# Performance work log

Hardware: AMD Instinct MI355X
Metric: run time of the kernel (lower is better)

The kernel has to match this reference:

```python
import jax, jax.numpy as jnp
import numpy as np

N = 4000; T_GRU = 32; T_TREE = 16; F = 256; HS = 128; H = 3 * HS; CC = 512; E = 64000; D4 = 4 * HS


def _gru_last(x, wi, wh, bi, bh):
    # x: [N, T, F]; torch GRU gate order r, z, n. Returns last hidden [N, H].
    xp = jnp.einsum('ntf,gf->ntg', x, wi) + bi  # [N, T, 3H]
    h0 = jnp.zeros((x.shape[0], wh.shape[1]), x.dtype)
    def step(h, xt):
        gh = h @ wh.T + bh
        ir, iz, inn = jnp.split(xt, 3, axis=1)
        hr, hz, hn = jnp.split(gh, 3, axis=1)
        r = jax.nn.sigmoid(ir + hr)
        z = jax.nn.sigmoid(iz + hz)
        n = jnp.tanh(inn + r * hn)
        return (1.0 - z) * n + z * h, None
    hT, _ = jax.lax.scan(step, h0, jnp.swapaxes(xp, 0, 1))
    return hT


def _tree_root(x, ioux_w, ioux_b, iouh_w, iouh_b, fx_w, fx_b, fh_w, fh_b):
    # Chain-structured TreeLSTM (each node has one child); x: [N, T, F], leaf-to-root.
    xi = jnp.einsum('ntf,gf->ntg', x, ioux_w) + ioux_b  # [N, T, 3M]
    xf = jnp.einsum('ntf,mf->ntm', x, fx_w) + fx_b      # [N, T, M]
    M = fh_w.shape[0]
    z0 = jnp.zeros((x.shape[0], M), x.dtype)
    def step(carry, xs):
        c, h = carry
        xi_t, xf_t = xs
        iou = xi_t + h @ iouh_w.T + iouh_b
        i, o, u = jnp.split(iou, 3, axis=1)
        f = jax.nn.sigmoid(xf_t + h @ fh_w.T + fh_b)
        c = jax.nn.sigmoid(i) * jnp.tanh(u) + f * c
        h = jax.nn.sigmoid(o) * jnp.tanh(c)
        return (c, h), None
    (c, h), _ = jax.lax.scan(step, (z0, z0), (jnp.swapaxes(xi, 0, 1), jnp.swapaxes(xf, 0, 1)))
    return h


def _gcn(x, w, b, row, col):
    # PyG GCNConv: self-loops + symmetric normalization.
    n = x.shape[0]
    xw = x @ w.T
    loops = jnp.arange(n, dtype=row.dtype)
    r = jnp.concatenate([row, loops])
    c = jnp.concatenate([col, loops])
    deg = jax.ops.segment_sum(jnp.ones(r.shape, x.dtype), c, num_segments=n)
    dinv = jnp.where(deg > 0, jax.lax.rsqrt(jnp.maximum(deg, 1e-12)), 0.0)
    norm = (dinv[r] * dinv[c])[:, None]
    return jax.ops.segment_sum(xw[r] * norm, c, num_segments=n) + b


def setup_inputs() -> dict:
    key = jax.random.key(0)
    ks = jax.random.split(key, 48)
    s = 0.05
    p = lambda i, sh: jax.random.normal(ks[i], sh, jnp.float32) * s
    return {
        'feat1': p(0, (N, T_GRU, F)),
        'feat2': p(1, (N, T_TREE, F)),
        'feat3': p(2, (N, T_TREE, F)),
        'feat4': p(3, (N, CC)),
        'edge_index': jax.random.randint(ks[4], (2, E), 0, N),
        'gru_wi': p(5, (3 * H, F)), 'gru_wh': p(6, (3 * H, H)),
        'gru_bi': p(7, (3 * H,)), 'gru_bh': p(8, (3 * H,)),
        't1_ioux_w': p(9, (3 * H, F)), 't1_ioux_b': p(10, (3 * H,)),
        't1_iouh_w': p(11, (3 * H, H)), 't1_iouh_b': p(12, (3 * H,)),
        't1_fx_w': p(13, (H, F)), 't1_fx_b': p(14, (H,)),
        't1_fh_w': p(15, (H, H)), 't1_fh_b': p(16, (H,)),
        't2_ioux_w': p(17, (3 * H, F)), 't2_ioux_b': p(18, (3 * H,)),
        't2_iouh_w': p(19, (3 * H, H)), 't2_iouh_b': p(20, (3 * H,)),
        't2_fx_w': p(21, (H, F)), 't2_fx_b': p(22, (H,)),
        't2_fh_w': p(23, (H, H)), 't2_fh_b': p(24, (H,)),
        'r1_w': p(25, (HS, H)), 'r1_b': p(26, (HS,)),
        'r2_w': p(27, (HS, H)), 'r2_b': p(28, (HS,)),
        'r3_w': p(29, (HS, H)), 'r3_b': p(30, (HS,)),
        'r4_w': p(31, (HS, CC)), 'r4_b': p(32, (HS,)),
        'gcn0_w': p(33, (D4, D4)), 'gcn0_b': p(34, (D4,)),
        'gcn1_w': p(35, (D4, D4)), 'gcn1_b': p(36, (D4,)),
        'r7_w': p(37, (2, D4)), 'r7_b': p(38, (2,)),
    }


def reference(feat1, feat2, feat3, feat4, edge_index,
              gru_wi, gru_wh, gru_bi, gru_bh,
              t1_ioux_w, t1_ioux_b, t1_iouh_w, t1_iouh_b, t1_fx_w, t1_fx_b, t1_fh_w, t1_fh_b,
              t2_ioux_w, t2_ioux_b, t2_iouh_w, t2_iouh_b, t2_fx_w, t2_fx_b, t2_fh_w, t2_fh_b,
              r1_w, r1_b, r2_w, r2_b, r3_w, r3_b, r4_w, r4_b,
              gcn0_w, gcn0_b, gcn1_w, gcn1_b, r7_w, r7_b):
    v1 = _gru_last(feat1, gru_wi, gru_wh, gru_bi, gru_bh)            # [N, H]
    v2 = _tree_root(feat2, t1_ioux_w, t1_ioux_b, t1_iouh_w, t1_iouh_b, t1_fx_w, t1_fx_b, t1_fh_w, t1_fh_b)
    v3 = _tree_root(feat3, t2_ioux_w, t2_ioux_b, t2_iouh_w, t2_iouh_b, t2_fx_w, t2_fx_b, t2_fh_w, t2_fh_b)
    f1 = v1 @ r1_w.T + r1_b
    f2 = v2 @ r2_w.T + r2_b
    f3 = v3 @ r3_w.T + r3_b
    f4 = feat4 @ r4_w.T + r4_b
    m = jnp.concatenate([f1, f2, f3, f4], axis=1)                    # [N, 4*HS]
    row, col = edge_index[0], edge_index[1]
    m = jax.nn.relu(_gcn(m, gcn0_w, gcn0_b, row, col))
    m = _gcn(m, gcn1_w, gcn1_b, row, col)
    m = jax.nn.softmax(m @ r7_w.T + r7_b, axis=1)                    # [N, 2]
    return m.T                                                       # [2, N]
```

## Files before the change

kernel.cpp:

```cpp
#include <hip/hip_runtime.h>
#include <hip/hip_bf16.h>
#include <math.h>

#define NN 4000
#define TG 32
#define TT 16
#define FF 256
#define HH 384
#define GCOLS 1536
#define KCAT 640
#define EE 64000
#define D4 512

typedef __attribute__((ext_vector_type(8))) short short8;
typedef __attribute__((ext_vector_type(4))) float float4v;

static __device__ __forceinline__ float fsig(float x)  { return 1.0f / (1.0f + __expf(-x)); }
static __device__ __forceinline__ float ftanh(float x) { return 2.0f / (1.0f + __expf(-2.0f*x)) - 1.0f; }
static __device__ __forceinline__ unsigned short f2bf(float f) {
    __hip_bfloat16 h = __float2bfloat16(f); return *reinterpret_cast<unsigned short*>(&h);
}

static __device__ __forceinline__ void async_copy16(const void* g, void* l) {
    __builtin_amdgcn_global_load_lds(
        (const __attribute__((address_space(1))) unsigned int*)g,
        (__attribute__((address_space(3))) unsigned int*)l, 16, 0, 0);
}

static __device__ __forceinline__ void xcd_swz(int& bx, int& by, int& bz) {
    const int gx = gridDim.x, gy = gridDim.y;
    const int nwg = gx * gy * gridDim.z;
    const int w = (blockIdx.z * gy + blockIdx.y) * gx + blockIdx.x;
    const int q = nwg >> 3, r = nwg & 7;
    const int xcd = w & 7, i = w >> 3;
    const int L = (xcd < r ? xcd*(q+1) : r*(q+1) + (xcd - r)*q) + i;
    bx = L % gx; int rest = L / gx;
    by = rest % gy; bz = rest / gy;
}

__global__ __launch_bounds__(256) void prep_w_kernel(
    const float* __restrict__ gwi, const float* __restrict__ gwh,
    const float* __restrict__ gbi, const float* __restrict__ gbh,
    const float* __restrict__ x1w, const float* __restrict__ x1b,
    const float* __restrict__ h1w, const float* __restrict__ h1b,
    const float* __restrict__ fx1w, const float* __restrict__ fx1b,
    const float* __restrict__ fh1w, const float* __restrict__ fh1b,
    const float* __restrict__ x2w, const float* __restrict__ x2b,
    const float* __restrict__ h2w, const float* __restrict__ h2b,
    const float* __restrict__ fx2w, const float* __restrict__ fx2b,
    const float* __restrict__ fh2w, const float* __restrict__ fh2b,
    __hip_bfloat16* __restrict__ Wx, __hip_bfloat16* __restrict__ Wh,
    float* __restrict__ bp)
{
    int z = blockIdx.z;
    int idx = blockIdx.x * 256 + threadIdx.x;
    int c = idx / KCAT, k = idx - c * KCAT;
    int bx = c >> 7, wc = (c >> 6) & 1, g = (c >> 4) & 3, rl = c & 15;
    int j = bx*32 + wc*16 + rl;
    float v = 0.0f, bv = 0.0f;
    if (z == 0) {
        if (g <= 1) {
            int row = g*HH + j;
            v = (k < FF) ? gwi[row*FF + k] : gwh[row*HH + (k-FF)];
            bv = gbi[row] + gbh[row];
        } else if (g == 2) {
            int row = 2*HH + j;
            v = (k < FF) ? gwi[row*FF + k] : 0.0f;
            bv = gbi[row];
        } else {
            int row = 2*HH + j;
            v = (k < FF) ? 0.0f : gwh[row*HH + (k-FF)];
            bv = gbh[row];
        }
    } else {
        const float* xw  = (z==1)? x1w  : x2w;   const float* xb  = (z==1)? x1b  : x2b;
        const float* hw  = (z==1)? h1w  : h2w;   const float* hb_ = (z==1)? h1b  : h2b;
        const float* fxw = (z==1)? fx1w : fx2w;  const float* fxb = (z==1)? fx1b : fx2b;
        const float* fhw = (z==1)? fh1w : fh2w;  const float* fhb = (z==1)? fh1b : fh2b;
        if (g < 3) {
            int row = g*HH + j;
            v = (k < FF) ? xw[row*FF + k] : hw[row*HH + (k-FF)];
            bv = xb[row] + hb_[row];
        } else {
            v = (k < FF) ? fxw[j*FF + k] : fhw[j*HH + (k-FF)];
            bv = fxb[j] + fhb[j];
        }
    }
    if (k < FF) Wx[(size_t)z*GCOLS*FF + (size_t)c*FF + k] = __float2bfloat16(v);
    else        Wh[(size_t)z*GCOLS*HH + (size_t)c*HH + (k-FF)] = __float2bfloat16(v);
    if (k == 0) bp[z*GCOLS + c] = bv;
}

__global__ __launch_bounds__(256) void f2b4_kernel(const float* __restrict__ s,
                                                   __hip_bfloat16* __restrict__ d, int n4)
{
    int i = blockIdx.x*256 + threadIdx.x;
    if (i >= n4) return;
    float4 v = ((const float4*)s)[i];
    ushort4 u = { f2bf(v.x), f2bf(v.y), f2bf(v.z), f2bf(v.w) };
    ((ushort4*)d)[i] = u;
}

#define BM 128
#define BN 128
#define BKK 32

__global__ __launch_bounds__(256) void gemm0_k(
    const __hip_bfloat16* __restrict__ Ab, size_t zA, int lda,
    const __hip_bfloat16* __restrict__ Wb, size_t zW, int K,
    const float* __restrict__ bias, size_t zB,
    float* __restrict__ C, size_t zC,
    __hip_bfloat16* __restrict__ C16, size_t zC16,
    int ldC, int M)
{
    const int z = blockIdx.z;
    const __hip_bfloat16* A = Ab + zA*z;
    const __hip_bfloat16* W = Wb + zW*z;

    __shared__ __align__(16) __hip_bfloat16 As[BM][BKK];
    __shared__ __align__(16) __hip_bfloat16 Bs[BN][BKK];

    const int tid  = threadIdx.x;
    const int lane = tid & 63;
    const int w    = tid >> 6;
    const int wr = w >> 1, wc = w & 1;
    const int rowBase = blockIdx.y * BM;
    const int colBase = blockIdx.x * BN;
    const int sRow = tid >> 2;
    const int sK   = (tid & 3) * 8;

    float4v acc[4][4];
    #pragma unroll
    for (int i = 0; i < 4; ++i)
        #pragma unroll
        for (int j = 0; j < 4; ++j)
            acc[i][j] = (float4v){0.f, 0.f, 0.f, 0.f};

    const int rl = lane & 15;
    const int kl = (lane >> 4) * 8;

    for (int kt = 0; kt < K; kt += BKK) {
        const int kk = kt + sK;
        #pragma unroll
        for (int i = 0; i < 2; ++i) {
            int gr = rowBase + i*64 + sRow;
            if (gr > M-1) gr = M-1;
            async_copy16(A + (size_t)gr*lda + kk, &As[i*64 + sRow][sK]);
        }
        #pragma unroll
        for (int i = 0; i < 2; ++i) {
            int r = i*64 + sRow;
            async_copy16(W + (size_t)(colBase + r)*K + kk, &Bs[r][sK]);
        }
        __syncthreads();

        short8 af[4], bfr[4];
        #pragma unroll
        for (int mi = 0; mi < 4; ++mi)
            af[mi] = *(const short8*)&As[wr*64 + mi*16 + rl][kl];
        #pragma unroll
        for (int ni = 0; ni < 4; ++ni)
            bfr[ni] = *(const short8*)&Bs[wc*64 + ni*16 + rl][kl];
        #pragma unroll
        for (int mi = 0; mi < 4; ++mi)
            #pragma unroll
            for (int ni = 0; ni < 4; ++ni)
                acc[mi][ni] = __builtin_amdgcn_mfma_f32_16x16x32_bf16(af[mi], bfr[ni], acc[mi][ni], 0, 0, 0);
        __syncthreads();
    }

    const int rq = (lane >> 4) * 4;
    float* Cz = C + zC*z;
    __hip_bfloat16* C16z = C16 ? (C16 + zC16*z) : nullptr;
    #pragma unroll
    for (int mi = 0; mi < 4; ++mi) {
        #pragma unroll
        for (int q = 0; q < 4; ++q) {
            int row = rowBase + wr*64 + mi*16 + rq + q;
            if (row >= M) continue;
            #pragma unroll
            for (int ni = 0; ni < 4; ++ni) {
                int col = colBase + wc*64 + ni*16 + rl;
                float v = acc[mi][ni][q];
                if (bias) v += bias[zB*z + col];
                Cz[(size_t)row*ldC + col] = v;
                if (C16z) C16z[(size_t)row*ldC + col] = __float2bfloat16(v);
            }
        }
    }
}

struct StepSet {
    const __hip_bfloat16 *X, *Hin, *Wx, *Wh;
    const float *bp, *Sin;
    float *Sout;
    __hip_bfloat16 *Hout;
    int lda, xoff;
};

#define NT (KCAT/BKK)
#define SBM 64

template<int MODE>
__global__ __launch_bounds__(256) void step_k(StepSet S)
{
    int bxi, byi, bzi;
    xcd_swz(bxi, byi, bzi);

    const __hip_bfloat16* X  = S.X;
    const __hip_bfloat16* Hi = S.Hin;
    const __hip_bfloat16* Wx = S.Wx;
    const __hip_bfloat16* Wh = S.Wh;
    const float* bp = S.bp;
    const float* Si = S.Sin;
    float* So = S.Sout;
    __hip_bfloat16* Ho = S.Hout;
    const int lda = S.lda, xoff = S.xoff;

    __shared__ __align__(16) __hip_bfloat16 As[4][SBM][BKK];
    __shared__ __align__(16) __hip_bfloat16 Bs[4][BN][BKK];

    const int tid  = threadIdx.x;
    const int lane = tid & 63;
    const int w    = tid >> 6;
    const int wr = w >> 1, wc = w & 1;
    const int rowBase = byi * SBM;
    const int colBase = bxi * BN;

    const int sR  = tid >> 2;
    const int sC  = tid & 3;
    const int sSw = sC ^ ((sR >> 1) & 3);
    int gra = rowBase + sR; if (gra > NN-1) gra = NN-1;

    auto stage = [&](int buf, int kt) {
        if (kt < FF) {
            const int kk = kt + sSw*8;
            async_copy16(X  + (size_t)gra*lda + xoff + kk,          &As[buf][sR][sC*8]);
            async_copy16(Wx + (size_t)(colBase + sR)*FF + kk,       &Bs[buf][sR][sC*8]);
            async_copy16(Wx + (size_t)(colBase + 64 + sR)*FF + kk,  &Bs[buf][64 + sR][sC*8]);
        } else {
            const int kk = kt - FF + sSw*8;
            async_copy16(Hi + (size_t)gra*HH + kk,                  &As[buf][sR][sC*8]);
            async_copy16(Wh + (size_t)(colBase + sR)*HH + kk,       &Bs[buf][sR][sC*8]);
            async_copy16(Wh + (size_t)(colBase + 64 + sR)*HH + kk,  &Bs[buf][64 + sR][sC*8]);
        }
    };

    float4v acc[2][4];
    #pragma unroll
    for (int i = 0; i < 2; ++i)
        #pragma unroll
        for (int j = 0; j < 4; ++j)
            acc[i][j] = (float4v){0.f, 0.f, 0.f, 0.f};

    const int rl = lane & 15;
    const int dF = (lane >> 4) ^ ((rl >> 1) & 3);

    stage(0, 0);
    stage(1, BKK);

    for (int it = 0; it < NT; ++it) {
        if (it < NT-1) asm volatile("s_waitcnt vmcnt(3)" ::: "memory");
        else           asm volatile("s_waitcnt vmcnt(0)" ::: "memory");
        __builtin_amdgcn_sched_barrier(0);
        __builtin_amdgcn_s_barrier();
        __builtin_amdgcn_sched_barrier(0);
        if (it + 2 < NT) stage((it+2)&3, (it+2)*BKK);
        __builtin_amdgcn_sched_barrier(0);

        const int cur = it & 3;
        short8 af[2], bfr[4];
        #pragma unroll
        for (int mi = 0; mi < 2; ++mi)
            af[mi] = *(const short8*)&As[cur][wr*32 + mi*16 + rl][dF*8];

        const bool xph = (it*BKK) < FF;
        if (MODE == 2) {
            #pragma unroll
            for (int ni = 0; ni < 4; ++ni)
                bfr[ni] = *(const short8*)&Bs[cur][wc*64 + ni*16 + rl][dF*8];
            asm volatile("s_waitcnt lgkmcnt(0)" ::: "memory");
            __builtin_amdgcn_sched_barrier(0);
            #pragma unroll
            for (int mi = 0; mi < 2; ++mi)
                #pragma unroll
                for (int ni = 0; ni < 4; ++ni)
                    acc[mi][ni] = __builtin_amdgcn_mfma_f32_16x16x32_bf16(af[mi], bfr[ni], acc[mi][ni], 0, 0, 0);
        } else if (xph) {
            #pragma unroll
            for (int ni = 0; ni < 3; ++ni)
                bfr[ni] = *(const short8*)&Bs[cur][wc*64 + ni*16 + rl][dF*8];
            asm volatile("s_waitcnt lgkmcnt(0)" ::: "memory");
            __builtin_amdgcn_sched_barrier(0);
            #pragma unroll
            for (int mi = 0; mi < 2; ++mi)
                #pragma unroll
                for (int ni = 0; ni < 3; ++ni)
                    acc[mi][ni] = __builtin_amdgcn_mfma_f32_16x16x32_bf16(af[mi], bfr[ni], acc[mi][ni], 0, 0, 0);
        } else {
            bfr[0] = *(const short8*)&Bs[cur][wc*64 + 0*16 + rl][dF*8];
            bfr[1] = *(const short8*)&Bs[cur][wc*64 + 1*16 + rl][dF*8];
            bfr[3] = *(const short8*)&Bs[cur][wc*64 + 3*16 + rl][dF*8];
            asm volatile("s_waitcnt lgkmcnt(0)" ::: "memory");
            __builtin_amdgcn_sched_barrier(0);
            #pragma unroll
            for (int mi = 0; mi < 2; ++mi) {
                acc[mi][0] = __builtin_amdgcn_mfma_f32_16x16x32_bf16(af[mi], bfr[0], acc[mi][0], 0, 0, 0);
                acc[mi][1] = __builtin_amdgcn_mfma_f32_16x16x32_bf16(af[mi], bfr[1], acc[mi][1], 0, 0, 0);
                acc[mi][3] = __builtin_amdgcn_mfma_f32_16x16x32_bf16(af[mi], bfr[3], acc[mi][3], 0, 0, 0);
            }
        }
    }

    const int rq = (lane >> 4) * 4;
    const int j  = (colBase >> 2) + wc*16 + rl;
    const int cb = colBase + wc*64 + rl;
    float b0 = bp[cb + 0];
    float b1 = bp[cb + 16];
    float b2 = bp[cb + 32];
    float b3 = bp[cb + 48];

    #pragma unroll
    for (int mi = 0; mi < 2; ++mi) {
        #pragma unroll
        for (int q = 0; q < 4; ++q) {
            int row = rowBase + wr*32 + mi*16 + rq + q;
            if (row >= NN) continue;
            float g0 = acc[mi][0][q] + b0;
            float g1 = acc[mi][1][q] + b1;
            float g2 = acc[mi][2][q] + b2;
            float g3 = acc[mi][3][q] + b3;
            size_t off = (size_t)row*HH + j;
            if (MODE == 1) {
                float r  = fsig(g0), zz = fsig(g1);
                float n  = ftanh(g2 + r*g3);
                float hp = Si[off];
                float hn = (1.0f - zz)*n + zz*hp;
                So[off] = hn;
                Ho[off] = __float2bfloat16(hn);
            } else {
                float cp = Si[off];
                float cn = fsig(g0)*ftanh(g2) + fsig(g3)*cp;
                So[off] = cn;
                float hn = fsig(g1)*ftanh(cn);
                Ho[off] = __float2bfloat16(hn);
            }
        }
    }
}

__global__ __launch_bounds__(256) void count_kernel(const int* __restrict__ col, int* __restrict__ degi)
{
    int e = blockIdx.x*256 + threadIdx.x;
    if (e < EE) atomicAdd(&degi[col[e]], 1);
}

__global__ __launch_bounds__(1024) void scan_kernel(const int* __restrict__ degi,
    int* __restrict__ start, int* __restrict__ cursor, float* __restrict__ dinv)
{
    __shared__ int s[1024];
    int t = threadIdx.x;
    int v[4]; int sum = 0;
    #pragma unroll
    for (int i = 0; i < 4; ++i) {
        int idx = t*4 + i;
        v[i] = (idx < NN) ? degi[idx] : 0;
        sum += v[i];
    }
    s[t] = sum;
    __syncthreads();
    for (int d = 1; d < 1024; d <<= 1) {
        int x = (t >= d) ? s[t-d] : 0;
        __syncthreads();
        s[t] += x;
        __syncthreads();
    }
    int base = s[t] - sum;
    int run = 0;
    #pragma unroll
    for (int i = 0; i < 4; ++i) {
        int idx = t*4 + i;
        if (idx < NN) {
            int st = base + run;
            start[idx] = st;
            cursor[idx] = st;
            dinv[idx] = rsqrtf((float)v[i] + 1.0f);
        }
        run += v[i];
    }
    if (t == 1023) start[NN] = s[1023];
}

__global__ __launch_bounds__(256) void fill_kernel(const int* __restrict__ row,
    const int* __restrict__ col, int* __restrict__ cursor, int* __restrict__ esrc)
{
    int e = blockIdx.x*256 + threadIdx.x;
    if (e < EE) {
        int c = col[e];
        int pos = atomicAdd(&cursor[c], 1);
        esrc[pos] = row[e];
    }
}

__global__ __launch_bounds__(256) void gather_kernel(const float* __restrict__ xw,
    const int* __restrict__ esrc, const int* __restrict__ start,
    const float* __restrict__ dinv, const float* __restrict__ bias,
    float* __restrict__ mout, __hip_bfloat16* __restrict__ mout16, int relu)
{
    int wv = threadIdx.x >> 6, lane = threadIdx.x & 63;
    int n = blockIdx.x*4 + wv;
    if (n >= NN) return;
    float a[8] = {0.f,0.f,0.f,0.f,0.f,0.f,0.f,0.f};
    int s0 = start[n], s1 = start[n+1];
    float dn = dinv[n];
    for (int e = s0; e < s1; ++e) {
        int r = esrc[e];
        float nrm = dinv[r]*dn;
        const float4 v0 = *(const float4*)(xw + (size_t)r*D4 + lane*8);
        const float4 v1 = *(const float4*)(xw + (size_t)r*D4 + lane*8 + 4);
        a[0] += v0.x*nrm; a[1] += v0.y*nrm; a[2] += v0.z*nrm; a[3] += v0.w*nrm;
        a[4] += v1.x*nrm; a[5] += v1.y*nrm; a[6] += v1.z*nrm; a[7] += v1.w*nrm;
    }
    const float4 u0 = *(const float4*)(xw + (size_t)n*D4 + lane*8);
    const float4 u1 = *(const float4*)(xw + (size_t)n*D4 + lane*8 + 4);
    float dd = dn*dn;
    float su[8] = {u0.x,u0.y,u0.z,u0.w,u1.x,u1.y,u1.z,u1.w};
    #pragma unroll
    for (int i = 0; i < 8; ++i) {
        float vv = a[i] + su[i]*dd + bias[lane*8 + i];
        if (relu) vv = fmaxf(vv, 0.0f);
        mout[(size_t)n*D4 + lane*8 + i] = vv;
        if (mout16) mout16[(size_t)n*D4 + lane*8 + i] = __float2bfloat16(vv);
    }
}

__global__ __launch_bounds__(256) void final_kernel(const float* __restrict__ m,
    const float* __restrict__ w, const float* __restrict__ b, float* __restrict__ out)
{
    int wave = threadIdx.x >> 6;
    int lane = threadIdx.x & 63;
    int n = blockIdx.x*4 + wave;
    const float* row = m + (size_t)n*D4 + lane*8;
    float4 v0 = *(const float4*)(row);
    float4 v1 = *(const float4*)(row + 4);
    const float* w0 = w + lane*8;
    const float* w1 = w + D4 + lane*8;
    float4 u0 = *(const float4*)(w0); float4 u1 = *(const float4*)(w0 + 4);
    float4 t0 = *(const float4*)(w1); float4 t1 = *(const float4*)(w1 + 4);
    float a = v0.x*u0.x + v0.y*u0.y + v0.z*u0.z + v0.w*u0.w
            + v1.x*u1.x + v1.y*u1.y + v1.z*u1.z + v1.w*u1.w;
    float bb = v0.x*t0.x + v0.y*t0.y + v0.z*t0.z + v0.w*t0.w
             + v1.x*t1.x + v1.y*t1.y + v1.z*t1.z + v1.w*t1.w;
    #pragma unroll
    for (int s = 32; s; s >>= 1) { a += __shfl_xor(a, s); bb += __shfl_xor(bb, s); }
    if (lane == 0) {
        float l0 = a + b[0], l1 = bb + b[1];
        float mx = fmaxf(l0, l1);
        float e0 = expf(l0 - mx), e1 = expf(l1 - mx);
        float s = e0 + e1;
        out[n]      = e0 / s;
        out[NN + n] = e1 / s;
    }
}

extern "C" void kernel_launch(void* const* d_in, const int* in_sizes, int n_in,
                              void* d_out, int out_size, void* d_ws, size_t ws_size,
                              hipStream_t stream)
{
    const float* feat1 = (const float*)d_in[0];
    const float* feat2 = (const float*)d_in[1];
    const float* feat3 = (const float*)d_in[2];
    const float* feat4 = (const float*)d_in[3];
    const int*   eidx  = (const int*)d_in[4];
    const float* r1w = (const float*)d_in[25]; const float* r1b = (const float*)d_in[26];
    const float* r2w = (const float*)d_in[27]; const float* r2b = (const float*)d_in[28];
    const float* r3w = (const float*)d_in[29]; const float* r3b = (const float*)d_in[30];
    const float* r4w = (const float*)d_in[31]; const float* r4b = (const float*)d_in[32];
    const float* g0w = (const float*)d_in[33]; const float* g0b = (const float*)d_in[34];
    const float* g1w = (const float*)d_in[35]; const float* g1b = (const float*)d_in[36];
    const float* r7w = (const float*)d_in[37]; const float* r7b = (const float*)d_in[38];

    float* ws = (float*)d_ws;
    size_t o = 0;
    auto alloc = [&](size_t nfl) { float* p = ws + o; o += (nfl + 3) & ~(size_t)3; return p; };

    float* hf0 = alloc((size_t)NN*HH);
    float* cf0 = alloc((size_t)2*NN*HH);
    __hip_bfloat16* hb0 = (__hip_bfloat16*)alloc((size_t)3*NN*HH/2);
    size_t zeroFloats = o;
    float* hf1 = alloc((size_t)NN*HH);
    float* cf1 = alloc((size_t)2*NN*HH);
    __hip_bfloat16* hb1 = (__hip_bfloat16*)alloc((size_t)3*NN*HH/2);
    __hip_bfloat16* xg  = (__hip_bfloat16*)alloc((size_t)TG*NN*FF/2);
    __hip_bfloat16* xt  = (__hip_bfloat16*)alloc((size_t)2*TT*NN*FF/2);
    __hip_bfloat16* Wx  = (__hip_bfloat16*)alloc((size_t)3*GCOLS*FF/2);
    __hip_bfloat16* Wh  = (__hip_bfloat16*)alloc((size_t)3*GCOLS*HH/2);
    float* bp   = alloc(3*GCOLS);
    float* mbuf = alloc((size_t)NN*D4);
    float* xwb  = alloc((size_t)NN*D4);
    float* dinv = alloc(NN);
    __hip_bfloat16* mbf16 = (__hip_bfloat16*)alloc((size_t)NN*D4/2);
    __hip_bfloat16* f4b   = (__hip_bfloat16*)alloc((size_t)NN*D4/2);
    __hip_bfloat16* rw123 = (__hip_bfloat16*)alloc((size_t)3*128*HH/2);
    float* rb123 = alloc(3*128);
    __hip_bfloat16* r4w16 = (__hip_bfloat16*)alloc((size_t)128*D4/2);
    __hip_bfloat16* g0w16 = (__hip_bfloat16*)alloc((size_t)D4*D4/2);
    __hip_bfloat16* g1w16 = (__hip_bfloat16*)alloc((size_t)D4*D4/2);
    int* degi   = (int*)alloc(NN);
    int* start  = (int*)alloc(NN + 4);
    int* cursor = (int*)alloc(NN);
    int* esrc   = (int*)alloc(EE);

    float* hfp[2] = {hf0, hf1};
    float* cfp[2] = {cf0, cf1};
    __hip_bfloat16* hbp[2] = {hb0, hb1};

    hipMemsetAsync(hf0, 0, zeroFloats*sizeof(float), stream);
    hipMemsetAsync(degi, 0, NN*sizeof(int), stream);

    prep_w_kernel<<<dim3(3840,1,3),256,0,stream>>>(
        (const float*)d_in[5],(const float*)d_in[6],(const float*)d_in[7],(const float*)d_in[8],
        (const float*)d_in[9],(const float*)d_in[10],(const float*)d_in[11],(const float*)d_in[12],
        (const float*)d_in[13],(const float*)d_in[14],(const float*)d_in[15],(const float*)d_in[16],
        (const float*)d_in[17],(const float*)d_in[18],(const float*)d_in[19],(const float*)d_in[20],
        (const float*)d_in[21],(const float*)d_in[22],(const float*)d_in[23],(const float*)d_in[24],
        Wx, Wh, bp);

    f2b4_kernel<<<32000,256,0,stream>>>(feat1, xg, TG*NN*FF/4);
    f2b4_kernel<<<16000,256,0,stream>>>(feat2, xt, TT*NN*FF/4);
    f2b4_kernel<<<16000,256,0,stream>>>(feat3, xt + (size_t)TT*NN*FF, TT*NN*FF/4);
    f2b4_kernel<<<2000,256,0,stream>>>(feat4, f4b, NN*D4/4);
    f2b4_kernel<<<48,256,0,stream>>>(r1w, rw123, 128*HH/4);
    f2b4_kernel<<<48,256,0,stream>>>(r2w, rw123 + 128*HH, 128*HH/4);
    f2b4_kernel<<<48,256,0,stream>>>(r3w, rw123 + 2*128*HH, 128*HH/4);
    f2b4_kernel<<<64,256,0,stream>>>(r4w, r4w16, 128*D4/4);
    f2b4_kernel<<<256,256,0,stream>>>(g0w, g0w16, D4*D4/4);
    f2b4_kernel<<<256,256,0,stream>>>(g1w, g1w16, D4*D4/4);
    hipMemcpyAsync(rb123,       r1b, 128*sizeof(float), hipMemcpyDeviceToDevice, stream);
    hipMemcpyAsync(rb123 + 128, r2b, 128*sizeof(float), hipMemcpyDeviceToDevice, stream);
    hipMemcpyAsync(rb123 + 256, r3b, 128*sizeof(float), hipMemcpyDeviceToDevice, stream);

    count_kernel<<<250,256,0,stream>>>(eidx + EE, degi);
    scan_kernel<<<1,1024,0,stream>>>(degi, start, cursor, dinv);
    fill_kernel<<<250,256,0,stream>>>(eidx, eidx + EE, cursor, esrc);

    for (int t = 0; t < TG; ++t) {
        int p = t & 1, q = p ^ 1;
        StepSet Gs = { xg, hbp[p], Wx, Wh, bp, hfp[p], hfp[q], hbp[q], TG*FF, t*FF };
        step_k<1><<<dim3(GCOLS/BN, 63, 1),256,0,stream>>>(Gs);
    }
    for (int t = 0; t < TT; ++t) {
        int p = t & 1, q = p ^ 1;
        for (int tr = 0; tr < 2; ++tr) {
            StepSet Ts = { xt + (size_t)tr*TT*NN*FF,
                           hbp[p] + (size_t)(1+tr)*NN*HH,
                           Wx + (size_t)(1+tr)*GCOLS*FF,
                           Wh + (size_t)(1+tr)*GCOLS*HH,
                           bp + (size_t)(1+tr)*GCOLS,
                           cfp[p] + (size_t)tr*NN*HH,
                           cfp[q] + (size_t)tr*NN*HH,
                           hbp[q] + (size_t)(1+tr)*NN*HH,
                           TT*FF, t*FF };
            step_k<2><<<dim3(GCOLS/BN, 63, 1),256,0,stream>>>(Ts);
        }
    }

    gemm0_k<<<dim3(1,32,3),256,0,stream>>>(
        hbp[0], (size_t)NN*HH, HH, rw123, (size_t)128*HH, HH, rb123, 128,
        mbuf, 128, mbf16, 128, D4, NN);
    gemm0_k<<<dim3(1,32,1),256,0,stream>>>(
        f4b, 0, D4, r4w16, 0, D4, r4b, 0,
        mbuf + 384, 0, mbf16 + 384, 0, D4, NN);

    gemm0_k<<<dim3(4,32,1),256,0,stream>>>(
        mbf16, 0, D4, g0w16, 0, D4, nullptr, 0,
        xwb, 0, nullptr, 0, D4, NN);
    gather_kernel<<<1000,256,0,stream>>>(xwb, esrc, start, dinv, g0b, mbuf, mbf16, 1);

    gemm0_k<<<dim3(4,32,1),256,0,stream>>>(
        mbf16, 0, D4, g1w16, 0, D4, nullptr, 0,
        xwb, 0, nullptr, 0, D4, NN);
    gather_kernel<<<1000,256,0,stream>>>(xwb, esrc, start, dinv, g1b, mbuf, nullptr, 0);

    final_kernel<<<1000,256,0,stream>>>(mbuf, r7w, r7b, (float*)d_out);
}
```

Before: 1.571 ms.

## Replace per-timestep recurrent kernel launches with persistent kernels using grid barriers

The GRU and both TreeLSTM recurrences now each run as one persistent kernel. Timesteps are separated by a hand-written grid-wide barrier that uses per-XCD atomic counters instead of 64 separate launches. This removes launch overhead and the inter-kernel drain at every timestep. It relies on all 756 blocks being co-resident (launch bounds raised to 3 blocks per CU), and a spin-wait barrier can deadlock if they are not. The barrier also adds atomic and sleep latency to every step.

```diff
diff --git a/kernel.cpp b/kernel.cpp
--- a/kernel.cpp
+++ b/kernel.cpp
@@ -36,6 +36,22 @@
     const int L = (xcd < r ? xcd*(q+1) : r*(q+1) + (xcd - r)*q) + i;
     bx = L % gx; int rest = L / gx;
     by = rest % gy; bz = rest / gy;
+}
+
+static __device__ __forceinline__ void gsync(int* sc, int step, int lx)
+{
+    __syncthreads();
+    if (threadIdx.x == 0) {
+        __threadfence();
+        const int per = 94 + (lx < 4 ? 1 : 0);
+        int v = __hip_atomic_fetch_add(sc + lx*16, 1, __ATOMIC_RELAXED, __HIP_MEMORY_SCOPE_AGENT);
+        if (v == per*(step+1) - 1)
+            __hip_atomic_fetch_add(sc + 128, 1, __ATOMIC_RELAXED, __HIP_MEMORY_SCOPE_AGENT);
+        while (__hip_atomic_load(sc + 128, __ATOMIC_RELAXED, __HIP_MEMORY_SCOPE_AGENT) < 8*(step+1))
+            __builtin_amdgcn_s_sleep(8);
+        __threadfence();
+    }
+    __syncthreads();
 }
 
 __global__ __launch_bounds__(256) void prep_w_kernel(
@@ -190,42 +206,24 @@
     }
 }
 
-struct StepSet {
-    const __hip_bfloat16 *X, *Hin, *Wx, *Wh;
-    const float *bp, *Sin;
-    float *Sout;
-    __hip_bfloat16 *Hout;
-    int lda, xoff;
-};
-
 #define NT (KCAT/BKK)
 #define SBM 64
 
 template<int MODE>
-__global__ __launch_bounds__(256) void step_k(StepSet S)
-{
-    int bxi, byi, bzi;
-    xcd_swz(bxi, byi, bzi);
-
-    const __hip_bfloat16* X  = S.X;
-    const __hip_bfloat16* Hi = S.Hin;
-    const __hip_bfloat16* Wx = S.Wx;
-    const __hip_bfloat16* Wh = S.Wh;
-    const float* bp = S.bp;
-    const float* Si = S.Sin;
-    float* So = S.Sout;
-    __hip_bfloat16* Ho = S.Hout;
-    const int lda = S.lda, xoff = S.xoff;
-
-    __shared__ __align__(16) __hip_bfloat16 As[4][SBM][BKK];
-    __shared__ __align__(16) __hip_bfloat16 Bs[4][BN][BKK];
-
+static __device__ __forceinline__ void step_body(
+    const __hip_bfloat16* __restrict__ X, int lda, int xoff,
+    const __hip_bfloat16* __restrict__ Hi,
+    const __hip_bfloat16* __restrict__ Wx, const __hip_bfloat16* __restrict__ Wh,
+    const float* __restrict__ bp,
+    const float* __restrict__ Si, float* __restrict__ So,
+    __hip_bfloat16* __restrict__ Ho,
+    __hip_bfloat16 (*As)[SBM][BKK], __hip_bfloat16 (*Bs)[BN][BKK],
+    int rowBase, int colBase)
+{
     const int tid  = threadIdx.x;
     const int lane = tid & 63;
     const int w    = tid >> 6;
     const int wr = w >> 1, wc = w & 1;
-    const int rowBase = byi * SBM;
-    const int colBase = bxi * BN;
 
     const int sR  = tid >> 2;
     const int sC  = tid & 3;
@@ -347,6 +345,63 @@
             }
         }
     }
+    asm volatile("s_waitcnt vmcnt(0)" ::: "memory");
+}
+
+__global__ __launch_bounds__(256, 3) void gru_persist(
+    const __hip_bfloat16* __restrict__ xg,
+    __hip_bfloat16* __restrict__ hbA, __hip_bfloat16* __restrict__ hbB,
+    float* __restrict__ hfA, float* __restrict__ hfB,
+    const __hip_bfloat16* __restrict__ Wx, const __hip_bfloat16* __restrict__ Wh,
+    const float* __restrict__ bp, int* __restrict__ sync)
+{
+    __shared__ __align__(16) __hip_bfloat16 As[4][SBM][BKK];
+    __shared__ __align__(16) __hip_bfloat16 Bs[4][BN][BKK];
+    int bxi, byi, bzi;
+    xcd_swz(bxi, byi, bzi);
+    const int lx = (blockIdx.y * gridDim.x + blockIdx.x) & 7;
+    const int rowBase = byi * SBM, colBase = bxi * BN;
+
+    for (int t = 0; t < TG; ++t) {
+        const int p = t & 1;
+        step_body<1>(xg, TG*FF, t*FF,
+                     p ? hbB : hbA, Wx, Wh, bp,
+                     p ? hfB : hfA, p ? hfA : hfB,
+                     p ? hbA : hbB,
+                     As, Bs, rowBase, colBase);
+        if (t < TG-1) gsync(sync, t, lx);
+    }
+}
+
+__global__ __launch_bounds__(256, 3) void tree_persist(
+    const __hip_bfloat16* __restrict__ xt,
+    __hip_bfloat16* __restrict__ hbA, __hip_bfloat16* __restrict__ hbB,
+    float* __restrict__ cfA, float* __restrict__ cfB,
+    const __hip_bfloat16* __restrict__ Wx, const __hip_bfloat16* __restrict__ Wh,
+    const float* __restrict__ bp, int* __restrict__ sync)
+{
+    __shared__ __align__(16) __hip_bfloat16 As[4][SBM][BKK];
+    __shared__ __align__(16) __hip_bfloat16 Bs[4][BN][BKK];
+    int bxi, byi, bzi;
+    xcd_swz(bxi, byi, bzi);
+    const int lx = (blockIdx.y * gridDim.x + blockIdx.x) & 7;
+    const int rowBase = byi * SBM, colBase = bxi * BN;
+
+    for (int t = 0; t < TT; ++t) {
+        const int p = t & 1;
+        for (int tr = 0; tr < 2; ++tr) {
+            step_body<2>(xt + (size_t)tr*TT*NN*FF, TT*FF, t*FF,
+                         (p ? hbB : hbA) + (size_t)tr*NN*HH,
+                         Wx + (size_t)tr*GCOLS*FF, Wh + (size_t)tr*GCOLS*HH,
+                         bp + (size_t)tr*GCOLS,
+                         (p ? cfB : cfA) + (size_t)tr*NN*HH,
+                         (p ? cfA : cfB) + (size_t)tr*NN*HH,
+                         (p ? hbA : hbB) + (size_t)tr*NN*HH,
+                         As, Bs, rowBase, colBase);
+            if (tr == 0) __syncthreads();
+        }
+        if (t < TT-1) gsync(sync, t, lx);
+    }
 }
 
 __global__ __launch_bounds__(256) void count_kernel(const int* __restrict__ col, int* __restrict__ degi)
@@ -510,13 +565,11 @@
     int* start  = (int*)alloc(NN + 4);
     int* cursor = (int*)alloc(NN);
     int* esrc   = (int*)alloc(EE);
-
-    float* hfp[2] = {hf0, hf1};
-    float* cfp[2] = {cf0, cf1};
-    __hip_bfloat16* hbp[2] = {hb0, hb1};
+    int* syncb  = (int*)alloc(512);
 
     hipMemsetAsync(hf0, 0, zeroFloats*sizeof(float), stream);
     hipMemsetAsync(degi, 0, NN*sizeof(int), stream);
+    hipMemsetAsync(syncb, 0, 512*sizeof(int), stream);
 
     prep_w_kernel<<<dim3(3840,1,3),256,0,stream>>>(
         (const float*)d_in[5],(const float*)d_in[6],(const float*)d_in[7],(const float*)d_in[8],
@@ -544,29 +597,15 @@
     scan_kernel<<<1,1024,0,stream>>>(degi, start, cursor, dinv);
     fill_kernel<<<250,256,0,stream>>>(eidx, eidx + EE, cursor, esrc);
 
-    for (int t = 0; t < TG; ++t) {
-        int p = t & 1, q = p ^ 1;
-        StepSet Gs = { xg, hbp[p], Wx, Wh, bp, hfp[p], hfp[q], hbp[q], TG*FF, t*FF };
-        step_k<1><<<dim3(GCOLS/BN, 63, 1),256,0,stream>>>(Gs);
-    }
-    for (int t = 0; t < TT; ++t) {
-        int p = t & 1, q = p ^ 1;
-        for (int tr = 0; tr < 2; ++tr) {
-            StepSet Ts = { xt + (size_t)tr*TT*NN*FF,
-                           hbp[p] + (size_t)(1+tr)*NN*HH,
-                           Wx + (size_t)(1+tr)*GCOLS*FF,
-                           Wh + (size_t)(1+tr)*GCOLS*HH,
-                           bp + (size_t)(1+tr)*GCOLS,
-                           cfp[p] + (size_t)tr*NN*HH,
-                           cfp[q] + (size_t)tr*NN*HH,
-                           hbp[q] + (size_t)(1+tr)*NN*HH,
-                           TT*FF, t*FF };
-            step_k<2><<<dim3(GCOLS/BN, 63, 1),256,0,stream>>>(Ts);
-        }
-    }
+    gru_persist<<<dim3(GCOLS/BN, 63, 1),256,0,stream>>>(
+        xg, hb0, hb1, hf0, hf1, Wx, Wh, bp, syncb);
+
+    tree_persist<<<dim3(GCOLS/BN, 63, 1),256,0,stream>>>(
+        xt, hb0 + (size_t)NN*HH, hb1 + (size_t)NN*HH, cf0, cf1,
+        Wx + (size_t)GCOLS*FF, Wh + (size_t)GCOLS*HH, bp + GCOLS, syncb + 256);
 
     gemm0_k<<<dim3(1,32,3),256,0,stream>>>(
-        hbp[0], (size_t)NN*HH, HH, rw123, (size_t)128*HH, HH, rb123, 128,
+        hb0, (size_t)NN*HH, HH, rw123, (size_t)128*HH, HH, rb123, 128,
         mbuf, 128, mbf16, 128, D4, NN);
     gemm0_k<<<dim3(1,32,1),256,0,stream>>>(
         f4b, 0, D4, r4w16, 0, D4, r4b, 0,
```

Result: slower. 3.035 ms (+93.1%).
